# Kernel tuning notes

Measured on AMD Instinct MI355X. Metric: run time of the kernel, lower is better.

## Reference

```python
import jax, jax.numpy as jnp
import numpy as np

N_NODES = 50000
N_EDGES = 800000
D_IN = 128
D_OUT = 128


def setup_inputs() -> dict:
    key = jax.random.key(0)
    ks = jax.random.split(key, 10)
    x = jax.random.normal(ks[0], (N_NODES, D_IN), dtype=jnp.float32)
    src = jax.random.randint(ks[1], (N_EDGES,), 0, N_NODES, dtype=jnp.int32)
    dst = jax.random.randint(ks[2], (N_EDGES,), 0, N_NODES, dtype=jnp.int32)
    s = 1.0 / np.sqrt(D_IN)
    def lin(k, din, dout):
        kw, kb = jax.random.split(k)
        W = jax.random.uniform(kw, (din, dout), minval=-s, maxval=s, dtype=jnp.float32)
        b = jax.random.uniform(kb, (dout,), minval=-s, maxval=s, dtype=jnp.float32)
        return W, b
    W1, b1 = lin(ks[3], D_IN, D_IN)
    W2, b2 = lin(ks[4], D_IN, D_IN)
    W3, b3 = lin(ks[5], D_IN, D_OUT)
    return dict(x=x, W1=W1, b1=b1, W2=W2, b2=b2, W3=W3, b3=b3, src=src, dst=dst)


def reference(x, W1, b1, W2, b2, W3, b3, src, dst):
    n = x.shape[0]
    ones = jnp.ones(src.shape[0], dtype=x.dtype)
    in_deg = jax.ops.segment_sum(ones, dst, num_segments=n)    # [N]
    out_deg = jax.ops.segment_sum(ones, src, num_segments=n)   # [N]

    def sage_gcn(h, W, b):
        # DGL SAGEConv(aggregator_type='gcn'), eval mode (feat_drop = identity):
        # h_neigh = (sum_{j in N(i)} h_j + h_i) / (in_deg_i + 1); out = h_neigh @ W + b
        neigh = jax.ops.segment_sum(h[src], dst, num_segments=n)  # [N, D]
        h_neigh = (neigh + h) / (in_deg + 1.0)[:, None]
        return h_neigh @ W + b

    h = sage_gcn(x, W1, b1)
    h = sage_gcn(h, W2, b2)

    # DGL GraphConv norm='both', allow_zero_in_degree=True:
    # out = D_in^{-1/2} A D_out^{-1/2} h W + b, degrees clamped to >= 1
    norm_out = jnp.clip(out_deg, 1.0) ** -0.5
    norm_in = jnp.clip(in_deg, 1.0) ** -0.5
    hs = h * norm_out[:, None]
    agg = jax.ops.segment_sum(hs[src], dst, num_segments=n)
    out = (agg * norm_in[:, None]) @ W3 + b3
    return out
```

## Files before the change

### kernel.cpp

```cpp
#include <hip/hip_runtime.h>

#define NN 50000
#define NE 800000
#define D 128

#define CH 128
#define EPC (NE / CH)
#define RGH 2
#define NPR2 (NN / RGH)
#define CSRCAP (NE + 4 * NN)

#define HIST_BLOCKS (CH * RGH)
#define CVT_BLOCKS 1563
#define WT_BLOCKS 48

typedef short bf16x8 __attribute__((ext_vector_type(8)));
typedef float f32x4 __attribute__((ext_vector_type(4)));


__device__ __forceinline__ unsigned bf16rne(float f) {
  unsigned u = __float_as_uint(f);
  return (u + 0x7fffu + ((u >> 16) & 1u)) >> 16;
}
__device__ __forceinline__ unsigned packbf(float lo, float hi) {
  return bf16rne(lo) | (bf16rne(hi) << 16);
}
__device__ __forceinline__ void bacc(float* a, uint4 u) {
  a[0] += __uint_as_float(u.x << 16);
  a[1] += __uint_as_float(u.x & 0xffff0000u);
  a[2] += __uint_as_float(u.y << 16);
  a[3] += __uint_as_float(u.y & 0xffff0000u);
  a[4] += __uint_as_float(u.z << 16);
  a[5] += __uint_as_float(u.z & 0xffff0000u);
  a[6] += __uint_as_float(u.w << 16);
  a[7] += __uint_as_float(u.w & 0xffff0000u);
}

__global__ __launch_bounds__(1024) void prep_kernel(
    const float* __restrict__ x, const float* __restrict__ W1,
    const float* __restrict__ W2, const float* __restrict__ W3,
    unsigned short* __restrict__ hbf, unsigned short* __restrict__ T1,
    unsigned short* __restrict__ T2, unsigned short* __restrict__ T3,
    const int* __restrict__ src, const int* __restrict__ dst,
    unsigned* __restrict__ partial) {
  __shared__ unsigned hcnt[NPR2];
  int b = blockIdx.x;
  int tid = threadIdx.x;
  if (b < HIST_BLOCKS) {
    int c = b >> 1;
    int r = b & 1;
    int base = r * NPR2;
    for (int i = tid; i < NPR2; i += 1024) hcnt[i] = 0;
    __syncthreads();
    int e0 = c * EPC;
    for (int i = tid; i < EPC; i += 1024) {
      int d = dst[e0 + i];
      int s = src[e0 + i];
      unsigned dr = (unsigned)(d - base);
      unsigned sr = (unsigned)(s - base);
      if (dr < NPR2) atomicAdd(&hcnt[dr], 1u);
      if (sr < NPR2) atomicAdd(&hcnt[sr], 0x10000u);
    }
    __syncthreads();
    for (int i = tid; i < NPR2; i += 1024)
      partial[(size_t)c * NN + base + i] = hcnt[i];
  } else if (b < HIST_BLOCKS + CVT_BLOCKS) {
    int i = (b - HIST_BLOCKS) * 1024 + tid;
    if (i < NN * D / 4) {
      float4 v = ((const float4*)x)[i];
      uint2 p;
      p.x = packbf(v.x, v.y);
      p.y = packbf(v.z, v.w);
      ((uint2*)hbf)[i] = p;
    }
  } else if (b < HIST_BLOCKS + CVT_BLOCKS + WT_BLOCKS) {
    int g = b - (HIST_BLOCKS + CVT_BLOCKS);
    int w = g >> 4;
    int i = (g & 15) * 1024 + tid;
    const float* W = (w == 0) ? W1 : (w == 1) ? W2 : W3;
    unsigned short* T = (w == 0) ? T1 : (w == 1) ? T2 : T3;
    int n = i >> 7, k = i & 127;
    T[n * 128 + k] = (unsigned short)bf16rne(W[k * 128 + n]);
  } else {
    if (tid < 16) ((uint4*)(hbf + (size_t)NN * D))[tid] = make_uint4(0, 0, 0, 0);
  }
}

__device__ __forceinline__ int block_excl_scan(int v, int* wsum) {
  int lane = threadIdx.x & 63;
  int w = threadIdx.x >> 6;
  int incl = v;
#pragma unroll
  for (int off = 1; off < 64; off <<= 1) {
    int t = __shfl_up(incl, off);
    if (lane >= off) incl += t;
  }
  if (lane == 63) wsum[w] = incl;
  __syncthreads();
  int wo = 0;
#pragma unroll
  for (int j = 0; j < 4; ++j)
    if (j < w) wo += wsum[j];
  return wo + incl - v;
}

__global__ __launch_bounds__(256) void degscan_kernel(const unsigned* __restrict__ partial,
                                                      unsigned short* __restrict__ pofs,
                                                      int* __restrict__ degtmp,
                                                      int* __restrict__ deg_out,
                                                      int* __restrict__ row_ptr,
                                                      int* __restrict__ partials, int N) {
  __shared__ int wsum[4];
  int d = blockIdx.x * 256 + threadIdx.x;
  int run = 0, ro = 0;
  if (d < N) {
#pragma unroll 8
    for (int c = 0; c < CH; ++c) {
      unsigned v = partial[(size_t)c * NN + d];
      pofs[(size_t)c * NN + d] = (unsigned short)run;
      run += (int)(v & 0xffffu);
      ro += (int)(v >> 16);
    }
    degtmp[d] = run;
    deg_out[d] = ro;
  }
  int pad = (run + 3) & ~3;
  int excl = block_excl_scan(pad, wsum);
  if (d <= N) row_ptr[d] = excl;
  if (threadIdx.x == 255) partials[blockIdx.x] = excl + pad;
}

__global__ __launch_bounds__(256) void scan2(int* __restrict__ partials, int nb) {
  __shared__ int wsum[4];
  int v = (threadIdx.x < nb) ? partials[threadIdx.x] : 0;
  int excl = block_excl_scan(v, wsum);
  if (threadIdx.x < nb) partials[threadIdx.x] = excl;
}

__global__ __launch_bounds__(1024) void fill_kernel(const int* __restrict__ src,
                                                    const int* __restrict__ dst,
                                                    const int* __restrict__ row_ptr,
                                                    const int* __restrict__ partials,
                                                    const unsigned short* __restrict__ pofs,
                                                    int* __restrict__ csr_src) {
  __shared__ int cur[NPR2];
  int tid = threadIdx.x;
  int c = blockIdx.x >> 1;
  int r = blockIdx.x & 1;
  int base = r * NPR2;
  for (int i = tid; i < NPR2; i += 1024) {
    int nd = base + i;
    cur[i] = row_ptr[nd] + partials[nd >> 8] + (int)pofs[(size_t)c * NN + nd];
  }
  __syncthreads();
  int e0 = c * EPC;
  for (int i = tid; i < EPC; i += 1024) {
    int d = dst[e0 + i];
    unsigned dr = (unsigned)(d - base);
    if (dr < NPR2) {
      int pos = atomicAdd(&cur[dr], 1);
      csr_src[pos] = src[e0 + i];
    }
  }
  if (c == CH - 1) {
    __syncthreads();
    for (int i = tid; i < NPR2; i += 1024) {
      int nd = base + i;
      int s = cur[i];
      int e = row_ptr[nd + 1] + partials[(nd + 1) >> 8];
      for (int j = s; j < e; ++j) csr_src[j] = NN;
    }
  }
}

template <int MODE>
__global__ __launch_bounds__(256, 8) void agg_kernel(const unsigned short* __restrict__ hb,
                                                     const int* __restrict__ row_ptr,
                                                     const int* __restrict__ partials,
                                                     const int* __restrict__ csr_src,
                                                     const int* __restrict__ degtmp,
                                                     unsigned short* __restrict__ outb, int N) {
  int qw = threadIdx.x >> 4;
  int col = threadIdx.x & 15;
  int node = blockIdx.x * 16 + qw;
  if (node >= N) return;
  int start = row_ptr[node] + partials[node >> 8];
  int end = row_ptr[node + 1] + partials[(node + 1) >> 8];
  int indeg = degtmp[node];
  uint4 srow = make_uint4(0, 0, 0, 0);
  if (MODE == 0) srow = ((const uint4*)(hb + (size_t)node * D))[col];
  float a0[8] = {0, 0, 0, 0, 0, 0, 0, 0};
  float a1[8] = {0, 0, 0, 0, 0, 0, 0, 0};
  const int* ce = csr_src + start;
  int cnt = end - start;
  for (int it = 0; it < cnt; it += 4) {
    int4 ix = *(const int4*)(ce + it);
    uint4 u0 = ((const uint4*)(hb + (size_t)ix.x * D))[col];
    uint4 u1 = ((const uint4*)(hb + (size_t)ix.y * D))[col];
    uint4 u2 = ((const uint4*)(hb + (size_t)ix.z * D))[col];
    uint4 u3 = ((const uint4*)(hb + (size_t)ix.w * D))[col];
    bacc(a0, u0);
    bacc(a1, u1);
    bacc(a0, u2);
    bacc(a1, u3);
  }
#pragma unroll
  for (int j = 0; j < 8; ++j) a0[j] += a1[j];
  if (MODE == 0) {
    float sf[8] = {0, 0, 0, 0, 0, 0, 0, 0};
    bacc(sf, srow);
    float inv = 1.0f / (float)(indeg + 1);
#pragma unroll
    for (int j = 0; j < 8; ++j) a0[j] = (a0[j] + sf[j]) * inv;
  } else {
    float sc = rsqrtf(fmaxf((float)indeg, 1.0f));
#pragma unroll
    for (int j = 0; j < 8; ++j) a0[j] *= sc;
  }
  uint4 p;
  p.x = packbf(a0[0], a0[1]);
  p.y = packbf(a0[2], a0[3]);
  p.z = packbf(a0[4], a0[5]);
  p.w = packbf(a0[6], a0[7]);
  ((uint4*)(outb + (size_t)node * D))[col] = p;
}

template <int MODE, int OUT_BF>
__global__ __launch_bounds__(256) void mgemm_kernel(const unsigned short* __restrict__ A,
                                                    const unsigned short* __restrict__ WT,
                                                    const float* __restrict__ bias,
                                                    const int* __restrict__ deg_out,
                                                    float* __restrict__ outf,
                                                    unsigned short* __restrict__ outb, int N) {
  __shared__ unsigned short sWT[128 * 136];
  int tid = threadIdx.x;
  for (int g = tid; g < 2048; g += 256) {
    int n = g >> 4, c = g & 15;
    uint4 v = ((const uint4*)WT)[g];
    *(uint4*)&sWT[n * 136 + c * 8] = v;
  }
  int wv = tid >> 6;
  int lane = tid & 63;
  int q = lane >> 4;
  int ln = lane & 15;
  int row0 = blockIdx.x * 64 + wv * 16;
  int arow = row0 + ln;
  if (arow >= N) arow = 0;
  const unsigned short* Ar = A + (size_t)arow * 128 + q * 8;
  bf16x8 af0 = *(const bf16x8*)(Ar + 0);
  bf16x8 af1 = *(const bf16x8*)(Ar + 32);
  bf16x8 af2 = *(const bf16x8*)(Ar + 64);
  bf16x8 af3 = *(const bf16x8*)(Ar + 96);
  f32x4 acc[8];
#pragma unroll
  for (int t = 0; t < 8; ++t) acc[t] = (f32x4){0.f, 0.f, 0.f, 0.f};
  __syncthreads();
#pragma unroll
  for (int t = 0; t < 8; ++t) {
    const unsigned short* Wr = &sWT[(t * 16 + ln) * 136 + q * 8];
    bf16x8 b0 = *(const bf16x8*)(Wr + 0);
    bf16x8 b1 = *(const bf16x8*)(Wr + 32);
    bf16x8 b2 = *(const bf16x8*)(Wr + 64);
    bf16x8 b3 = *(const bf16x8*)(Wr + 96);
    acc[t] = __builtin_amdgcn_mfma_f32_16x16x32_bf16(af0, b0, acc[t], 0, 0, 0);
    acc[t] = __builtin_amdgcn_mfma_f32_16x16x32_bf16(af1, b1, acc[t], 0, 0, 0);
    acc[t] = __builtin_amdgcn_mfma_f32_16x16x32_bf16(af2, b2, acc[t], 0, 0, 0);
    acc[t] = __builtin_amdgcn_mfma_f32_16x16x32_bf16(af3, b3, acc[t], 0, 0, 0);
  }
  float scl[4];
#pragma unroll
  for (int r = 0; r < 4; ++r) {
    scl[r] = 1.0f;
    if (MODE == 1) {
      int row = row0 + q * 4 + r;
      int rr = (row < N) ? row : 0;
      scl[r] = rsqrtf(fmaxf((float)deg_out[rr], 1.0f));
    }
  }
#pragma unroll
  for (int t = 0; t < 8; ++t) {
    float b = bias[t * 16 + ln];
#pragma unroll
    for (int r = 0; r < 4; ++r) {
      int row = row0 + q * 4 + r;
      if (row < N) {
        float v = (acc[t][r] + b) * scl[r];
        if (OUT_BF)
          outb[(size_t)row * 128 + t * 16 + ln] = (unsigned short)bf16rne(v);
        else
          outf[(size_t)row * 128 + t * 16 + ln] = v;
      }
    }
  }
}


extern "C" void kernel_launch(void* const* d_in, const int* in_sizes, int n_in,
                              void* d_out, int out_size, void* d_ws, size_t ws_size,
                              hipStream_t stream) {
  const float* x = (const float*)d_in[0];
  const float* W1 = (const float*)d_in[1];
  const float* b1 = (const float*)d_in[2];
  const float* W2 = (const float*)d_in[3];
  const float* b2 = (const float*)d_in[4];
  const float* W3 = (const float*)d_in[5];
  const float* b3 = (const float*)d_in[6];
  const int* src = (const int*)d_in[7];
  const int* dst = (const int*)d_in[8];
  float* out = (float*)d_out;

  const int N = NN;

  unsigned short* hbf = (unsigned short*)d_ws;
  unsigned short* WT1 = hbf + (size_t)(NN + 1) * D;
  unsigned short* WT2 = WT1 + D * D;
  unsigned short* WT3 = WT2 + D * D;
  int* degtmp = (int*)(WT3 + D * D);
  int* deg_out = degtmp + NN;
  int* row_ptr = deg_out + NN;
  int* partials = row_ptr + NN + 4;
  int* csr_src = partials + 256;
  unsigned* partial = (unsigned*)(csr_src + CSRCAP);
  unsigned short* pofs = (unsigned short*)(partial + (size_t)CH * NN);
  unsigned short* aggB = (unsigned short*)partial;

  const int scanBlocks = (N + 255) / 256;

  prep_kernel<<<HIST_BLOCKS + CVT_BLOCKS + WT_BLOCKS + 1, 1024, 0, stream>>>(
      x, W1, W2, W3, hbf, WT1, WT2, WT3, src, dst, partial);
  degscan_kernel<<<scanBlocks, 256, 0, stream>>>(partial, pofs, degtmp, deg_out,
                                                 row_ptr, partials, N);
  scan2<<<1, 256, 0, stream>>>(partials, scanBlocks);
  fill_kernel<<<HIST_BLOCKS, 1024, 0, stream>>>(src, dst, row_ptr, partials, pofs,
                                                csr_src);

  int aggBlocks = (N + 15) / 16;
  int gemmBlocks = (N + 63) / 64;

  agg_kernel<0><<<aggBlocks, 256, 0, stream>>>(hbf, row_ptr, partials, csr_src, degtmp,
                                               aggB, N);
  mgemm_kernel<0, 1><<<gemmBlocks, 256, 0, stream>>>(aggB, WT1, b1, deg_out, nullptr, hbf, N);
  agg_kernel<0><<<aggBlocks, 256, 0, stream>>>(hbf, row_ptr, partials, csr_src, degtmp,
                                               aggB, N);
  mgemm_kernel<1, 1><<<gemmBlocks, 256, 0, stream>>>(aggB, WT2, b2, deg_out, nullptr, hbf, N);
  agg_kernel<1><<<aggBlocks, 256, 0, stream>>>(hbf, row_ptr, partials, csr_src, degtmp,
                                               aggB, N);
  mgemm_kernel<0, 0><<<gemmBlocks, 256, 0, stream>>>(aggB, WT3, b3, deg_out, out, nullptr, N);
}
```

Measured before the change: 268.0 us.

## Parallelize per-node chunk scan across 16 lanes and halve histogram chunk count

The serial per-node loop over histogram chunks is replaced by a kernel where 16 lanes each handle 4 chunks and combine their partial sums with a segmented shuffle scan. The row-pointer scan moves into a separate kernel that reads the computed degrees. The chunk count drops from 128 to 64, which halves the partial-histogram traffic but gives each histogram block twice as many edges. The change adds one kernel launch, and the per-node global accesses become strided across chunks rather than coalesced across nodes.

```diff
diff --git a/kernel.cpp b/kernel.cpp
--- a/kernel.cpp
+++ b/kernel.cpp
@@ -4,7 +4,7 @@
 #define NE 800000
 #define D 128
 
-#define CH 128
+#define CH 64
 #define EPC (NE / CH)
 #define RGH 2
 #define NPR2 (NN / RGH)
@@ -86,6 +86,41 @@
   }
 }
 
+__global__ __launch_bounds__(256) void pdegscan_kernel(const unsigned* __restrict__ partial,
+                                                       unsigned short* __restrict__ pofs,
+                                                       int* __restrict__ degtmp,
+                                                       int* __restrict__ deg_out) {
+  int tid = threadIdx.x;
+  int node_i = tid >> 4;
+  int tc = tid & 15;
+  int d = blockIdx.x * 16 + node_i;
+  int c0 = tc * 4;
+  unsigned v0 = partial[(size_t)(c0 + 0) * NN + d];
+  unsigned v1 = partial[(size_t)(c0 + 1) * NN + d];
+  unsigned v2 = partial[(size_t)(c0 + 2) * NN + d];
+  unsigned v3 = partial[(size_t)(c0 + 3) * NN + d];
+  int d0 = (int)(v0 & 0xffffu), d1 = (int)(v1 & 0xffffu);
+  int d2 = (int)(v2 & 0xffffu), d3 = (int)(v3 & 0xffffu);
+  int tsum = d0 + d1 + d2 + d3;
+  int ssum = (int)(v0 >> 16) + (int)(v1 >> 16) + (int)(v2 >> 16) + (int)(v3 >> 16);
+  int incl = tsum, incs = ssum;
+#pragma unroll
+  for (int off = 1; off < 16; off <<= 1) {
+    int t0 = __shfl_up(incl, off, 16);
+    int t1 = __shfl_up(incs, off, 16);
+    if (tc >= off) { incl += t0; incs += t1; }
+  }
+  int excl = incl - tsum;
+  pofs[(size_t)(c0 + 0) * NN + d] = (unsigned short)excl;
+  pofs[(size_t)(c0 + 1) * NN + d] = (unsigned short)(excl + d0);
+  pofs[(size_t)(c0 + 2) * NN + d] = (unsigned short)(excl + d0 + d1);
+  pofs[(size_t)(c0 + 3) * NN + d] = (unsigned short)(excl + d0 + d1 + d2);
+  if (tc == 15) {
+    degtmp[d] = incl;
+    deg_out[d] = incs;
+  }
+}
+
 __device__ __forceinline__ int block_excl_scan(int v, int* wsum) {
   int lane = threadIdx.x & 63;
   int w = threadIdx.x >> 6;
@@ -104,26 +139,12 @@
   return wo + incl - v;
 }
 
-__global__ __launch_bounds__(256) void degscan_kernel(const unsigned* __restrict__ partial,
-                                                      unsigned short* __restrict__ pofs,
-                                                      int* __restrict__ degtmp,
-                                                      int* __restrict__ deg_out,
+__global__ __launch_bounds__(256) void rowscan_kernel(const int* __restrict__ degtmp,
                                                       int* __restrict__ row_ptr,
                                                       int* __restrict__ partials, int N) {
   __shared__ int wsum[4];
   int d = blockIdx.x * 256 + threadIdx.x;
-  int run = 0, ro = 0;
-  if (d < N) {
-#pragma unroll 8
-    for (int c = 0; c < CH; ++c) {
-      unsigned v = partial[(size_t)c * NN + d];
-      pofs[(size_t)c * NN + d] = (unsigned short)run;
-      run += (int)(v & 0xffffu);
-      ro += (int)(v >> 16);
-    }
-    degtmp[d] = run;
-    deg_out[d] = ro;
-  }
+  int run = (d < N) ? degtmp[d] : 0;
   int pad = (run + 3) & ~3;
   int excl = block_excl_scan(pad, wsum);
   if (d <= N) row_ptr[d] = excl;
@@ -328,8 +349,8 @@
 
   prep_kernel<<<HIST_BLOCKS + CVT_BLOCKS + WT_BLOCKS + 1, 1024, 0, stream>>>(
       x, W1, W2, W3, hbf, WT1, WT2, WT3, src, dst, partial);
-  degscan_kernel<<<scanBlocks, 256, 0, stream>>>(partial, pofs, degtmp, deg_out,
-                                                 row_ptr, partials, N);
+  pdegscan_kernel<<<NN / 16, 256, 0, stream>>>(partial, pofs, degtmp, deg_out);
+  rowscan_kernel<<<scanBlocks, 256, 0, stream>>>(degtmp, row_ptr, partials, N);
   scan2<<<1, 256, 0, stream>>>(partials, scanBlocks);
   fill_kernel<<<HIST_BLOCKS, 1024, 0, stream>>>(src, dst, row_ptr, partials, pofs,
                                                 csr_src);
```

After: 271.7 us. No clear change (+1.4%).
